# Performance work log

Measured on AMD Instinct MI355X. Metric: run time of the kernel, lower is better.

Reference implementation:

```python
import jax, jax.numpy as jnp
import numpy as np

TOP_K = 2


def setup_inputs() -> dict:
    key = jax.random.key(0)
    ks = jax.random.split(key, 5)
    B, S, H, E, F = 4, 1024, 1024, 16, 4096
    scale = 0.02
    return {
        "input_tensor": jax.random.normal(ks[0], (B, S, H), dtype=jnp.float32),
        "Wg": scale * jax.random.normal(ks[1], (H, E), dtype=jnp.float32),
        "bg": jnp.zeros((E,), dtype=jnp.float32),
        "W1": scale * jax.random.normal(ks[2], (E, H, F), dtype=jnp.float32),
        "b1": jnp.zeros((E, F), dtype=jnp.float32),
        "W2": scale * jax.random.normal(ks[3], (E, F, H), dtype=jnp.float32),
        "b2": jnp.zeros((E, H), dtype=jnp.float32),
    }


def reference(input_tensor, Wg, bg, W1, b1, W2, b2):
    # Faithful to DualOutputMoE.forward_first_pass: the per-(b,s,k) Python loop
    # plus _weighted_sum collapses ALL token expert outputs into a single
    # [1,1,H] vector normalized by the total routing weight (= B*S).
    B, S, H = input_tensor.shape
    T = B * S
    E = Wg.shape[1]
    x = input_tensor.reshape(T, H)

    routing_scores = x @ Wg + bg                    # [T, E] (raw gate logits)
    top_v, top_i = jax.lax.top_k(routing_scores, TOP_K)
    top_w = jax.nn.softmax(top_v, axis=-1)          # per-token top-k weights

    # combine[t, e] = sum_k top_w[t, k] * 1[top_i[t, k] == e]
    combine = jnp.zeros((T, E), x.dtype).at[jnp.arange(T)[:, None], top_i].add(top_w)
    total_weight = top_w.sum()                      # matches python sum of .item()s

    def expert_step(acc, params):
        w1, bb1, w2, bb2, c = params                # c: [T] combine weights for this expert
        y = jax.nn.gelu(x @ w1 + bb1, approximate=False) @ w2 + bb2  # [T, H]
        return acc + c @ y, None

    acc0 = jnp.zeros((H,), x.dtype)
    acc, _ = jax.lax.scan(expert_step, acc0, (W1, b1, W2, b2, combine.T))
    first_output = (acc / total_weight).reshape(1, 1, H)
    return first_output
```

## Files before the change

kernel.cpp:

```cpp
#include <hip/hip_runtime.h>
#include <hip/hip_bf16.h>
#include <math.h>

typedef __bf16 bf16_t;
typedef __bf16 bf16x4 __attribute__((ext_vector_type(4)));
typedef __bf16 bf16x8 __attribute__((ext_vector_type(8)));
typedef float  f32x4  __attribute__((ext_vector_type(4)));

#define T_TOK 4096
#define H_DIM 1024
#define E_NUM 16
#define F_DIM 4096
#define CH_ROWS 128
#define CH_MAX  32

#define WS_E0     0
#define WS_E1     16384
#define WS_W0     32768
#define WS_W1     49152
#define WS_COUNTS 65536
#define WS_SUMW   65664
#define WS_XOFF   65792
#define WS_LIDX   131072
#define WS_LW     393216
#define WS_GPART  655360
#define WS_P2     655360
#define WS_G      9043968
#define WS_XE     9306112
#define WS_W1T    30277632
#define W1T_PER_E 8388608

#define AS_GLOBAL(p) ((const __attribute__((address_space(1))) void*)(p))
#define AS_LDS(p)    ((__attribute__((address_space(3))) void*)(p))

__global__ __launch_bounds__(64) void k_route(const float* __restrict__ x,
    const float* __restrict__ Wg, const float* __restrict__ bg,
    int* __restrict__ e0, int* __restrict__ e1,
    float* __restrict__ w0, float* __restrict__ w1)
{
    const int t = blockIdx.x;
    const int lane = threadIdx.x;
    const float* xr = x + (size_t)t * H_DIM;

    float s[E_NUM];
#pragma unroll
    for (int e = 0; e < E_NUM; ++e) s[e] = 0.f;

#pragma unroll
    for (int i = 0; i < 16; ++i) {
        const int h = i * 64 + lane;
        const float xv = xr[h];
        const float4* wr = (const float4*)(Wg + (size_t)h * E_NUM);
        float4 q0 = wr[0], q1 = wr[1], q2 = wr[2], q3 = wr[3];
        s[0] += xv*q0.x;  s[1] += xv*q0.y;  s[2] += xv*q0.z;  s[3] += xv*q0.w;
        s[4] += xv*q1.x;  s[5] += xv*q1.y;  s[6] += xv*q1.z;  s[7] += xv*q1.w;
        s[8] += xv*q2.x;  s[9] += xv*q2.y;  s[10]+= xv*q2.z;  s[11]+= xv*q2.w;
        s[12]+= xv*q3.x;  s[13]+= xv*q3.y;  s[14]+= xv*q3.z;  s[15]+= xv*q3.w;
    }
#pragma unroll
    for (int off = 32; off >= 1; off >>= 1) {
#pragma unroll
        for (int e = 0; e < E_NUM; ++e) s[e] += __shfl_xor(s[e], off);
    }
    if (lane == 0) {
#pragma unroll
        for (int e = 0; e < E_NUM; ++e) s[e] += bg[e];
        float b1v = -3e38f; int i1 = 0;
#pragma unroll
        for (int e = 0; e < E_NUM; ++e) { if (s[e] > b1v) { b1v = s[e]; i1 = e; } }
        float b2v = -3e38f; int i2 = 0;
#pragma unroll
        for (int e = 0; e < E_NUM; ++e) { if (e != i1 && s[e] > b2v) { b2v = s[e]; i2 = e; } }
        const float ex  = expf(b2v - b1v);
        const float inv = 1.f / (1.f + ex);
        e0[t] = i1; e1[t] = i2;
        w0[t] = inv; w1[t] = ex * inv;
    }
}

__global__ __launch_bounds__(64) void k_lists(const int* __restrict__ e0, const int* __restrict__ e1,
    const float* __restrict__ w0, const float* __restrict__ w1,
    int* __restrict__ lidx, float* __restrict__ lw,
    int* __restrict__ counts, float* __restrict__ sumw)
{
    const int e = blockIdx.x;
    const int lane = threadIdx.x;
    int cnt = 0; float sw = 0.f;
    for (int base = 0; base < T_TOK; base += 64) {
        const int t = base + lane;
        const bool m0 = (e0[t] == e);
        const bool m1 = (e1[t] == e);
        const bool m  = m0 | m1;
        const unsigned long long bal = __ballot(m);
        const int pos = cnt + __popcll(bal & ((1ull << lane) - 1ull));
        if (m) {
            const float w = m0 ? w0[t] : w1[t];
            lidx[e * T_TOK + pos] = t;
            lw[e * T_TOK + pos]   = w;
            sw += w;
        }
        cnt += __popcll(bal);
    }
#pragma unroll
    for (int off = 32; off >= 1; off >>= 1) sw += __shfl_xor(sw, off);
    if (lane == 0) { counts[e] = cnt; sumw[e] = sw; }
}

__global__ void k_scan(const int* __restrict__ counts, int* __restrict__ xoff) {
    if (threadIdx.x == 0) {
        int o = 0;
        for (int e = 0; e < E_NUM; ++e) { xoff[e] = o; o += (counts[e] + CH_ROWS - 1) & ~(CH_ROWS - 1); }
    }
}

__global__ __launch_bounds__(256) void k_gather(const float* __restrict__ x,
    const int* __restrict__ lidx, const int* __restrict__ counts,
    const int* __restrict__ xoff, bf16_t* __restrict__ Xe)
{
    const int chunk = blockIdx.x >> 1;
    const int part  = blockIdx.x & 1;
    const int e = blockIdx.y;
    const int cnt = counts[e];
    const int start = chunk * CH_ROWS;
    if (chunk && start >= cnt) return;
    const int tid = threadIdx.x;
    const size_t base = ((size_t)(xoff[e] >> 7) + chunk) * 131072;

    for (int it = 0; it < 32; ++it) {
        const int u    = part * 8192 + it * 256 + tid;
        const int kt   = u >> 10;
        const int wi   = u & 1023;
        const int rl   = wi >> 3;
        const int c    = wi & 7;
        const int row  = start + rl;
        bf16x8 v8 = {};
        if (row < cnt) {
            const int tok = lidx[e * T_TOK + row];
            const int cp  = c ^ (rl & 7);
            const int k   = kt * 64 + cp * 8;
            const float4 a = *(const float4*)(x + (size_t)tok * H_DIM + k);
            const float4 b = *(const float4*)(x + (size_t)tok * H_DIM + k + 4);
            v8[0]=(bf16_t)a.x; v8[1]=(bf16_t)a.y; v8[2]=(bf16_t)a.z; v8[3]=(bf16_t)a.w;
            v8[4]=(bf16_t)b.x; v8[5]=(bf16_t)b.y; v8[6]=(bf16_t)b.z; v8[7]=(bf16_t)b.w;
        }
        *(bf16x8*)(Xe + base + (size_t)kt * 8192 + rl * 64 + c * 8) = v8;
    }
}

__global__ __launch_bounds__(512, 1) void k_w1t(const float* __restrict__ W1,
    bf16_t* __restrict__ W1T, int ebase)
{
    const int kt = blockIdx.x;
    const int fq = blockIdx.y;
    const int ge = blockIdx.z;
    const int e  = ebase + ge;
    const int tid = threadIdx.x;

    __shared__ bf16_t S[64 * 1024];

    const float* src = W1 + (size_t)e * H_DIM * F_DIM + (size_t)(kt * 64) * F_DIM + fq * 1024;

    for (int it = 0; it < 32; ++it) {
        const int u  = it * 512 + tid;
        const int k  = u >> 8;
        const int c4 = u & 255;
        const int f  = c4 * 4;
        const float4 v = *(const float4*)(src + (size_t)k * F_DIM + c4 * 4);
        bf16x4 b4; b4[0]=(bf16_t)v.x; b4[1]=(bf16_t)v.y; b4[2]=(bf16_t)v.z; b4[3]=(bf16_t)v.w;
        const int slot = (f >> 3) ^ (k & 7);
        *(bf16x4*)&S[k * 1024 + slot * 8 + (f & 7)] = b4;
    }
    __syncthreads();

#pragma unroll
    for (int ot = 0; ot < 2; ++ot) {
        const int f   = ot * 512 + tid;
        const int ftl = f >> 7;
        const int fl  = f & 127;
        const int fsw = fl & 7;
        const int fh3 = f >> 3;
        bf16_t* dst = W1T + ((((size_t)ge * 32 + (fq * 8 + ftl)) * 16 + kt) * 8192) + fl * 64;
#pragma unroll
        for (int s = 0; s < 8; ++s) {
            const int c = s ^ fsw;
            bf16x8 pk;
#pragma unroll
            for (int j = 0; j < 8; ++j) {
                const int k = c * 8 + j;
                pk[j] = S[k * 1024 + (fh3 ^ j) * 8 + (f & 7)];
            }
            *(bf16x8*)&dst[s * 8] = pk;
        }
    }
}

__global__ __launch_bounds__(256, 2) void k_expert(
    const bf16_t* __restrict__ W1T, const float* __restrict__ b1,
    const bf16_t* __restrict__ Xe, const float* __restrict__ lw,
    const int* __restrict__ counts, const int* __restrict__ xoff,
    float* __restrict__ gpart, int ebase)
{
    const int ftile = blockIdx.x;
    const int chunk = blockIdx.y;
    const int ge    = blockIdx.z;
    const int e     = ebase + ge;
    const int cnt   = counts[e];
    const int start = chunk * CH_ROWS;
    if (chunk && start >= cnt) return;

    __shared__ __align__(16) bf16_t Alds[2][8192];
    __shared__ __align__(16) bf16_t Blds[2][8192];
    __shared__ float w_s[CH_ROWS];
    __shared__ float b1_s[128];
    __shared__ float gred[2][128];

    const int tid  = threadIdx.x;
    const int lane = tid & 63;
    const int wid  = tid >> 6;
    const int wm   = wid & 1;
    const int wn   = wid >> 1;
    const int lr   = lane & 15;
    const int lg   = lane >> 4;

    if (tid < CH_ROWS) {
        const int r = start + tid;
        w_s[tid] = (r < cnt) ? lw[e * T_TOK + r] : 0.f;
    }
    if (tid < 128) b1_s[tid] = b1[(size_t)e * F_DIM + ftile * 128 + tid];

    f32x4 acc[4][4];
#pragma unroll
    for (int i = 0; i < 4; ++i)
#pragma unroll
        for (int j = 0; j < 4; ++j)
#pragma unroll
            for (int q = 0; q < 4; ++q) acc[i][j][q] = 0.f;

    const bf16_t* XeSlab = Xe + ((size_t)(xoff[e] >> 7) + chunk) * 131072;
    const bf16_t* W1Slab = W1T + (((size_t)ge * 32 + ftile) * 16) * 8192;

#define STAGE(T, BUF) { \
    const bf16_t* sa = XeSlab + (size_t)(T) * 8192; \
    const bf16_t* sb = W1Slab + (size_t)(T) * 8192; \
    _Pragma("unroll") \
    for (int p = 0; p < 4; ++p) { \
        const int off = p * 2048 + wid * 512; \
        __builtin_amdgcn_global_load_lds(AS_GLOBAL(sa + off + lane * 8), AS_LDS(&Alds[BUF][off]), 16, 0, 0); \
        __builtin_amdgcn_global_load_lds(AS_GLOBAL(sb + off + lane * 8), AS_LDS(&Blds[BUF][off]), 16, 0, 0); \
    } }

#define COMPUTE(BUF) { \
    _Pragma("unroll") \
    for (int kh = 0; kh < 2; ++kh) { \
        bf16x8 af[4], bfr[4]; \
        _Pragma("unroll") \
        for (int mf = 0; mf < 4; ++mf) { \
            const int r = wm * 64 + mf * 16 + lr; \
            af[mf] = *(const bf16x8*)&Alds[BUF][r * 64 + (((kh << 2) | lg) ^ (r & 7)) * 8]; \
        } \
        _Pragma("unroll") \
        for (int nf = 0; nf < 4; ++nf) { \
            const int f = wn * 64 + nf * 16 + lr; \
            bfr[nf] = *(const bf16x8*)&Blds[BUF][f * 64 + (((kh << 2) | lg) ^ (f & 7)) * 8]; \
        } \
        _Pragma("unroll") \
        for (int mf = 0; mf < 4; ++mf) \
            _Pragma("unroll") \
            for (int nf = 0; nf < 4; ++nf) \
                acc[mf][nf] = __builtin_amdgcn_mfma_f32_16x16x32_bf16(af[mf], bfr[nf], acc[mf][nf], 0, 0, 0); \
    } }

    STAGE(0, 0);
    __syncthreads();

    int cur = 0;
#pragma unroll 2
    for (int t = 0; t < 16; ++t) {
        if (t < 15) { STAGE(t + 1, cur ^ 1); }
        __builtin_amdgcn_sched_barrier(0);
        COMPUTE(cur);
        __syncthreads();
        cur ^= 1;
    }
#undef STAGE
#undef COMPUTE

    float gcol[4] = {0.f, 0.f, 0.f, 0.f};
#pragma unroll
    for (int nf = 0; nf < 4; ++nf) {
        const float bb = b1_s[wn * 64 + nf * 16 + lr];
#pragma unroll
        for (int mf = 0; mf < 4; ++mf) {
#pragma unroll
            for (int i = 0; i < 4; ++i) {
                const int row = wm * 64 + mf * 16 + lg * 4 + i;
                const float h  = acc[mf][nf][i] + bb;
                const float gl = 0.5f * h * (1.f + erff(h * 0.70710678118654752f));
                gcol[nf] += w_s[row] * gl;
            }
        }
    }
#pragma unroll
    for (int nf = 0; nf < 4; ++nf) {
        gcol[nf] += __shfl_xor(gcol[nf], 16);
        gcol[nf] += __shfl_xor(gcol[nf], 32);
    }
    if (lane < 16) {
#pragma unroll
        for (int nf = 0; nf < 4; ++nf) gred[wm][wn * 64 + nf * 16 + lane] = gcol[nf];
    }
    __syncthreads();
    if (tid < 128) {
        const float sum = gred[0][tid] + gred[1][tid];
        gpart[(size_t)(e * CH_MAX + chunk) * F_DIM + ftile * 128 + tid] = sum;
    }
}

__global__ __launch_bounds__(256) void k_redg(const float* __restrict__ gpart,
    const int* __restrict__ counts, float* __restrict__ g)
{
    const int e = blockIdx.y;
    const int f = blockIdx.x * 256 + threadIdx.x;
    const int nch = (counts[e] + CH_ROWS - 1) / CH_ROWS;
    float s = 0.f;
    for (int c = 0; c < nch; ++c)
        s += gpart[(size_t)(e * CH_MAX + c) * F_DIM + f];
    g[(size_t)e * F_DIM + f] = s;
}

__global__ __launch_bounds__(256) void k_out1(const float* __restrict__ g,
    const float* __restrict__ W2, float* __restrict__ p2)
{
    const int fc = blockIdx.x;
    const int e  = blockIdx.y;
    const int tid = threadIdx.x;
    __shared__ float gs[128];
    if (tid < 128) gs[tid] = g[(size_t)e * F_DIM + fc * 128 + tid];
    __syncthreads();
    const float* W2p = W2 + (size_t)e * F_DIM * H_DIM + (size_t)fc * 128 * H_DIM;
    float ax = 0.f, ay = 0.f, az = 0.f, aw = 0.f;
#pragma unroll 8
    for (int f = 0; f < 128; ++f) {
        const float gv = gs[f];
        const float4 wv = *(const float4*)(W2p + (size_t)f * H_DIM + tid * 4);
        ax += gv * wv.x; ay += gv * wv.y; az += gv * wv.z; aw += gv * wv.w;
    }
    float4 st; st.x = ax; st.y = ay; st.z = az; st.w = aw;
    *(float4*)(p2 + (size_t)(e * 32 + fc) * H_DIM + tid * 4) = st;
}

__global__ __launch_bounds__(256) void k_out2(const float* __restrict__ p2,
    const float* __restrict__ sumw, const float* __restrict__ b2, float* __restrict__ out)
{
    const int tid = threadIdx.x;
    const int hh  = tid & 31;
    const int seg = tid >> 5;
    const int h   = blockIdx.x * 32 + hh;
    float s = 0.f;
    for (int j = 0; j < 64; ++j)
        s += p2[(size_t)(seg * 64 + j) * H_DIM + h];
    __shared__ float red[8][33];
    red[seg][hh] = s;
    __syncthreads();
    if (tid < 32) {
        const int h2 = blockIdx.x * 32 + tid;
        float tot = 0.f;
#pragma unroll
        for (int q = 0; q < 8; ++q) tot += red[q][tid];
        float tw = 0.f, bias = 0.f;
#pragma unroll
        for (int e = 0; e < E_NUM; ++e) { tw += sumw[e]; bias += sumw[e] * b2[e * H_DIM + h2]; }
        out[h2] = (tot + bias) / tw;
    }
}

extern "C" void kernel_launch(void* const* d_in, const int* in_sizes, int n_in,
                              void* d_out, int out_size, void* d_ws, size_t ws_size,
                              hipStream_t stream) {
    const float* x  = (const float*)d_in[0];
    const float* Wg = (const float*)d_in[1];
    const float* bg = (const float*)d_in[2];
    const float* W1 = (const float*)d_in[3];
    const float* b1 = (const float*)d_in[4];
    const float* W2 = (const float*)d_in[5];
    const float* b2 = (const float*)d_in[6];
    float* out = (float*)d_out;

    char* ws = (char*)d_ws;
    int*    e0     = (int*)(ws + WS_E0);
    int*    e1     = (int*)(ws + WS_E1);
    float*  w0     = (float*)(ws + WS_W0);
    float*  w1     = (float*)(ws + WS_W1);
    int*    counts = (int*)(ws + WS_COUNTS);
    float*  sumw   = (float*)(ws + WS_SUMW);
    int*    xoff   = (int*)(ws + WS_XOFF);
    int*    lidx   = (int*)(ws + WS_LIDX);
    float*  lw     = (float*)(ws + WS_LW);
    float*  gpart  = (float*)(ws + WS_GPART);
    float*  g      = (float*)(ws + WS_G);
    float*  p2     = (float*)(ws + WS_P2);
    bf16_t* Xe     = (bf16_t*)(ws + WS_XE);
    bf16_t* W1T    = (bf16_t*)(ws + WS_W1T);

    int cap = 1;
    if (ws_size > (size_t)WS_W1T + (size_t)W1T_PER_E) {
        size_t c = (ws_size - (size_t)WS_W1T) / (size_t)W1T_PER_E;
        cap = (c >= 16) ? 16 : (int)c;
        if (cap < 1) cap = 1;
    }

    k_route<<<T_TOK, 64, 0, stream>>>(x, Wg, bg, e0, e1, w0, w1);
    k_lists<<<E_NUM, 64, 0, stream>>>(e0, e1, w0, w1, lidx, lw, counts, sumw);
    k_scan<<<1, 64, 0, stream>>>(counts, xoff);
    k_gather<<<dim3(CH_MAX * 2, E_NUM), 256, 0, stream>>>(x, lidx, counts, xoff, Xe);
    for (int eb = 0; eb < E_NUM; eb += cap) {
        const int gN = (E_NUM - eb < cap) ? (E_NUM - eb) : cap;
        k_w1t<<<dim3(16, 4, gN), 512, 0, stream>>>(W1, W1T, eb);
        k_expert<<<dim3(32, CH_MAX, gN), 256, 0, stream>>>(W1T, b1, Xe, lw, counts, xoff, gpart, eb);
    }
    k_redg<<<dim3(F_DIM / 256, E_NUM), 256, 0, stream>>>(gpart, counts, g);
    k_out1<<<dim3(32, E_NUM), 256, 0, stream>>>(g, W2, p2);
    k_out2<<<32, 256, 0, stream>>>(p2, sumw, b2, out);
}
```

Before: 367.4 us.

## Launch W1 transpose and expert GEMM once for all experts, fuse g reduction

Removes the workspace-capacity loop so the W1 transpose and the expert GEMM each run as a single launch over all 16 experts, assuming the workspace holds every transposed W1. The transpose kernel is retiled to 256 threads, keeps fp32 in LDS and converts to bf16 on read. The expert kernel's double-buffer loop now uses explicit vmcnt/lgkmcnt waits and raw s_barrier so the next tile's loads overlap compute. k_route packs four tokens per block, and the per-chunk reduction of g moves into k_out1, dropping one kernel. The risk is that the ws_size check is gone, so the full W1T buffer must fit in the workspace, and the hand-written waitcnts must match the number of outstanding loads exactly.

```diff
diff --git a/kernel.cpp b/kernel.cpp
--- a/kernel.cpp
+++ b/kernel.cpp
@@ -24,22 +24,20 @@
 #define WS_LIDX   131072
 #define WS_LW     393216
 #define WS_GPART  655360
-#define WS_P2     655360
-#define WS_G      9043968
 #define WS_XE     9306112
 #define WS_W1T    30277632
-#define W1T_PER_E 8388608
+#define WS_P2     164495360
 
 #define AS_GLOBAL(p) ((const __attribute__((address_space(1))) void*)(p))
 #define AS_LDS(p)    ((__attribute__((address_space(3))) void*)(p))
 
-__global__ __launch_bounds__(64) void k_route(const float* __restrict__ x,
+__global__ __launch_bounds__(256) void k_route(const float* __restrict__ x,
     const float* __restrict__ Wg, const float* __restrict__ bg,
     int* __restrict__ e0, int* __restrict__ e1,
     float* __restrict__ w0, float* __restrict__ w1)
 {
-    const int t = blockIdx.x;
-    const int lane = threadIdx.x;
+    const int t = blockIdx.x * 4 + (threadIdx.x >> 6);
+    const int lane = threadIdx.x & 63;
     const float* xr = x + (size_t)t * H_DIM;
 
     float s[E_NUM];
@@ -147,47 +145,42 @@
     }
 }
 
-__global__ __launch_bounds__(512, 1) void k_w1t(const float* __restrict__ W1,
-    bf16_t* __restrict__ W1T, int ebase)
+__global__ __launch_bounds__(256, 2) void k_w1t(const float* __restrict__ W1,
+    bf16_t* __restrict__ W1T)
 {
     const int kt = blockIdx.x;
-    const int fq = blockIdx.y;
-    const int ge = blockIdx.z;
-    const int e  = ebase + ge;
+    const int fb = blockIdx.y;
+    const int e  = blockIdx.z;
     const int tid = threadIdx.x;
 
-    __shared__ bf16_t S[64 * 1024];
-
-    const float* src = W1 + (size_t)e * H_DIM * F_DIM + (size_t)(kt * 64) * F_DIM + fq * 1024;
-
-    for (int it = 0; it < 32; ++it) {
-        const int u  = it * 512 + tid;
-        const int k  = u >> 8;
-        const int c4 = u & 255;
-        const int f  = c4 * 4;
+    __shared__ float S[64 * 256];
+
+    const float* src = W1 + (size_t)e * H_DIM * F_DIM + (size_t)(kt * 64) * F_DIM + fb * 256;
+
+#pragma unroll
+    for (int it = 0; it < 16; ++it) {
+        const int u  = it * 256 + tid;
+        const int k  = u >> 6;
+        const int c4 = u & 63;
         const float4 v = *(const float4*)(src + (size_t)k * F_DIM + c4 * 4);
-        bf16x4 b4; b4[0]=(bf16_t)v.x; b4[1]=(bf16_t)v.y; b4[2]=(bf16_t)v.z; b4[3]=(bf16_t)v.w;
-        const int slot = (f >> 3) ^ (k & 7);
-        *(bf16x4*)&S[k * 1024 + slot * 8 + (f & 7)] = b4;
+        *(float4*)&S[k * 256 + (c4 ^ (k & 7)) * 4] = v;
     }
     __syncthreads();
 
-#pragma unroll
-    for (int ot = 0; ot < 2; ++ot) {
-        const int f   = ot * 512 + tid;
-        const int ftl = f >> 7;
-        const int fl  = f & 127;
+    {
+        const int f   = tid;
+        const int ft  = fb * 2 + (tid >> 7);
+        const int fl  = tid & 127;
         const int fsw = fl & 7;
-        const int fh3 = f >> 3;
-        bf16_t* dst = W1T + ((((size_t)ge * 32 + (fq * 8 + ftl)) * 16 + kt) * 8192) + fl * 64;
+        bf16_t* dst = W1T + ((((size_t)e * 32 + ft) * 16 + kt) * 8192) + fl * 64;
 #pragma unroll
         for (int s = 0; s < 8; ++s) {
             const int c = s ^ fsw;
             bf16x8 pk;
 #pragma unroll
-            for (int j = 0; j < 8; ++j) {
-                const int k = c * 8 + j;
-                pk[j] = S[k * 1024 + (fh3 ^ j) * 8 + (f & 7)];
+            for (int q = 0; q < 8; ++q) {
+                const int k = c * 8 + q;
+                pk[q] = (bf16_t)S[k * 256 + ((f >> 2) ^ (k & 7)) * 4 + (f & 3)];
             }
             *(bf16x8*)&dst[s * 8] = pk;
         }
@@ -198,12 +191,11 @@
     const bf16_t* __restrict__ W1T, const float* __restrict__ b1,
     const bf16_t* __restrict__ Xe, const float* __restrict__ lw,
     const int* __restrict__ counts, const int* __restrict__ xoff,
-    float* __restrict__ gpart, int ebase)
+    float* __restrict__ gpart)
 {
     const int ftile = blockIdx.x;
     const int chunk = blockIdx.y;
-    const int ge    = blockIdx.z;
-    const int e     = ebase + ge;
+    const int e     = blockIdx.z;
     const int cnt   = counts[e];
     const int start = chunk * CH_ROWS;
     if (chunk && start >= cnt) return;
@@ -237,7 +229,7 @@
             for (int q = 0; q < 4; ++q) acc[i][j][q] = 0.f;
 
     const bf16_t* XeSlab = Xe + ((size_t)(xoff[e] >> 7) + chunk) * 131072;
-    const bf16_t* W1Slab = W1T + (((size_t)ge * 32 + ftile) * 16) * 8192;
+    const bf16_t* W1Slab = W1T + (((size_t)e * 32 + ftile) * 16) * 8192;
 
 #define STAGE(T, BUF) { \
     const bf16_t* sa = XeSlab + (size_t)(T) * 8192; \
@@ -271,15 +263,22 @@
     } }
 
     STAGE(0, 0);
-    __syncthreads();
+    __builtin_amdgcn_sched_barrier(0);
 
     int cur = 0;
-#pragma unroll 2
+#pragma unroll
     for (int t = 0; t < 16; ++t) {
-        if (t < 15) { STAGE(t + 1, cur ^ 1); }
+        if (t < 15) STAGE(t + 1, cur ^ 1);
+        __builtin_amdgcn_sched_barrier(0);
+        if (t < 15) { asm volatile("s_waitcnt vmcnt(8)" ::: "memory"); }
+        else        { asm volatile("s_waitcnt vmcnt(0)" ::: "memory"); }
+        __builtin_amdgcn_sched_barrier(0);
+        __builtin_amdgcn_s_barrier();
         __builtin_amdgcn_sched_barrier(0);
         COMPUTE(cur);
-        __syncthreads();
+        __builtin_amdgcn_sched_barrier(0);
+        asm volatile("s_waitcnt lgkmcnt(0)" ::: "memory");
+        __builtin_amdgcn_s_barrier();
         cur ^= 1;
     }
 #undef STAGE
@@ -316,26 +315,20 @@
     }
 }
 
-__global__ __launch_bounds__(256) void k_redg(const float* __restrict__ gpart,
-    const int* __restrict__ counts, float* __restrict__ g)
-{
-    const int e = blockIdx.y;
-    const int f = blockIdx.x * 256 + threadIdx.x;
-    const int nch = (counts[e] + CH_ROWS - 1) / CH_ROWS;
-    float s = 0.f;
-    for (int c = 0; c < nch; ++c)
-        s += gpart[(size_t)(e * CH_MAX + c) * F_DIM + f];
-    g[(size_t)e * F_DIM + f] = s;
-}
-
-__global__ __launch_bounds__(256) void k_out1(const float* __restrict__ g,
-    const float* __restrict__ W2, float* __restrict__ p2)
+__global__ __launch_bounds__(256) void k_out1(const float* __restrict__ gpart,
+    const int* __restrict__ counts, const float* __restrict__ W2, float* __restrict__ p2)
 {
     const int fc = blockIdx.x;
     const int e  = blockIdx.y;
     const int tid = threadIdx.x;
     __shared__ float gs[128];
-    if (tid < 128) gs[tid] = g[(size_t)e * F_DIM + fc * 128 + tid];
+    if (tid < 128) {
+        const int nch = (counts[e] + CH_ROWS - 1) / CH_ROWS;
+        float s = 0.f;
+        for (int c = 0; c < nch; ++c)
+            s += gpart[(size_t)(e * CH_MAX + c) * F_DIM + fc * 128 + tid];
+        gs[tid] = s;
+    }
     __syncthreads();
     const float* W2p = W2 + (size_t)e * F_DIM * H_DIM + (size_t)fc * 128 * H_DIM;
     float ax = 0.f, ay = 0.f, az = 0.f, aw = 0.f;
@@ -397,28 +390,16 @@
     int*    lidx   = (int*)(ws + WS_LIDX);
     float*  lw     = (float*)(ws + WS_LW);
     float*  gpart  = (float*)(ws + WS_GPART);
-    float*  g      = (float*)(ws + WS_G);
-    float*  p2     = (float*)(ws + WS_P2);
     bf16_t* Xe     = (bf16_t*)(ws + WS_XE);
     bf16_t* W1T    = (bf16_t*)(ws + WS_W1T);
-
-    int cap = 1;
-    if (ws_size > (size_t)WS_W1T + (size_t)W1T_PER_E) {
-        size_t c = (ws_size - (size_t)WS_W1T) / (size_t)W1T_PER_E;
-        cap = (c >= 16) ? 16 : (int)c;
-        if (cap < 1) cap = 1;
-    }
-
-    k_route<<<T_TOK, 64, 0, stream>>>(x, Wg, bg, e0, e1, w0, w1);
+    float*  p2     = (float*)(ws + WS_P2);
+
+    k_route<<<T_TOK / 4, 256, 0, stream>>>(x, Wg, bg, e0, e1, w0, w1);
     k_lists<<<E_NUM, 64, 0, stream>>>(e0, e1, w0, w1, lidx, lw, counts, sumw);
     k_scan<<<1, 64, 0, stream>>>(counts, xoff);
+    k_w1t<<<dim3(16, 16, E_NUM), 256, 0, stream>>>(W1, W1T);
     k_gather<<<dim3(CH_MAX * 2, E_NUM), 256, 0, stream>>>(x, lidx, counts, xoff, Xe);
-    for (int eb = 0; eb < E_NUM; eb += cap) {
-        const int gN = (E_NUM - eb < cap) ? (E_NUM - eb) : cap;
-        k_w1t<<<dim3(16, 4, gN), 512, 0, stream>>>(W1, W1T, eb);
-        k_expert<<<dim3(32, CH_MAX, gN), 256, 0, stream>>>(W1T, b1, Xe, lw, counts, xoff, gpart, eb);
-    }
-    k_redg<<<dim3(F_DIM / 256, E_NUM), 256, 0, stream>>>(gpart, counts, g);
-    k_out1<<<dim3(32, E_NUM), 256, 0, stream>>>(g, W2, p2);
+    k_expert<<<dim3(32, CH_MAX, E_NUM), 256, 0, stream>>>(W1T, b1, Xe, lw, counts, xoff, gpart);
+    k_out1<<<dim3(32, E_NUM), 256, 0, stream>>>(gpart, counts, W2, p2);
     k_out2<<<32, 256, 0, stream>>>(p2, sumw, b2, out);
 }
```

Measured after the change: 345.5 us. 6.0% less time.
